# Kernel tuning notes

Measured on AMD Instinct MI355X. Metric: run time of the kernel, lower is better.

The kernel has to match this reference:

```python
import jax, jax.numpy as jnp
import numpy as np

N_NODES = 50000
N_EDGES = 800000
F_IN = 128
HEADS = 4
C_OUT = 16
NEG_SLOPE = 0.2


def setup_inputs() -> dict:
    key = jax.random.key(0)
    k1, k2, k3, k4, k5 = jax.random.split(key, 5)
    x = jax.random.normal(k1, (N_NODES, F_IN), dtype=jnp.float32)
    edge_index = jax.random.randint(k2, (2, N_EDGES), 0, N_NODES, dtype=jnp.int64)
    W = jax.random.normal(k3, (F_IN, HEADS * C_OUT), dtype=jnp.float32) * (1.0 / np.sqrt(F_IN))
    att_src = jax.random.normal(k4, (HEADS, C_OUT), dtype=jnp.float32) * (1.0 / np.sqrt(C_OUT))
    att_dst = jax.random.normal(k5, (HEADS, C_OUT), dtype=jnp.float32) * (1.0 / np.sqrt(C_OUT))
    bias = jnp.zeros((HEADS * C_OUT,), dtype=jnp.float32)
    return {"x": x, "edge_index": edge_index, "W": W,
            "att_src": att_src, "att_dst": att_dst, "bias": bias}


def reference(x, edge_index, W, att_src, att_dst, bias):
    N = x.shape[0]
    H, C = att_src.shape
    # PyG GATConv default: add self-loops
    loop = jnp.arange(N, dtype=edge_index.dtype)
    ei = jnp.concatenate([edge_index, jnp.stack([loop, loop])], axis=1)  # [2, E+N]
    src, dst = ei[0], ei[1]

    h = (x @ W).reshape(N, H, C)                      # [N, H, C]
    a_src = jnp.einsum('nhc,hc->nh', h, att_src)      # [N, H]
    a_dst = jnp.einsum('nhc,hc->nh', h, att_dst)      # [N, H]

    e = a_src[src] + a_dst[dst]                       # [E+N, H]
    e = jnp.where(e > 0, e, NEG_SLOPE * e)            # leaky_relu(0.2)

    # segment softmax over destination node (every segment has a self-loop)
    m = jax.ops.segment_max(e, dst, num_segments=N)   # [N, H]
    e = jnp.exp(e - m[dst])
    s = jax.ops.segment_sum(e, dst, num_segments=N)   # [N, H]
    alpha = e / (s[dst] + 1e-16)                      # [E+N, H]

    # scatter-aggregate weighted neighbor features
    out = jax.ops.segment_sum(h[src] * alpha[..., None], dst, num_segments=N)  # [N, H, C]
    out = out.reshape(N, H * C) + bias                # concat heads + bias
    return out, alpha
```

## Files before the change

### kernel.cpp

```cpp
#include <hip/hip_runtime.h>

#define N_NODES 50000
#define N_EDGES 800000
#define EN      (N_EDGES + N_NODES)
#define F_IN    128
#define HC      64
#define NEG_SLOPE 0.2f
#define NBUCK   196
#define BCAP    5120
#define P3_EPB  4096
#define LIN_BLOCKS 782
#define NBLK    196
#define RCAP    64
#define NSLOT   (NBLK * RCAP)
#define XPAD    136

typedef __attribute__((ext_vector_type(8))) short bf16x8;
typedef __attribute__((ext_vector_type(4))) float f32x4;

static __device__ __forceinline__ unsigned short f2bf(float f) {
    unsigned int b = __float_as_uint(f);
    return (unsigned short)((b + 0x7FFFu + ((b >> 16) & 1u)) >> 16);
}

__global__ __launch_bounds__(256) void
kA_linear_bin(const float* __restrict__ x, const float* __restrict__ W,
              const float* __restrict__ att_src, const float* __restrict__ att_dst,
              const int* __restrict__ ei,
              unsigned short* __restrict__ hbf, float* __restrict__ a_src,
              float* __restrict__ a_dst, int* __restrict__ bins,
              int* __restrict__ cntg) {
    __shared__ unsigned short xs[64][XPAD];
    __shared__ unsigned short wt[64][XPAD];
    __shared__ int bcnt_l[NBUCK];
    const int tid = threadIdx.x;

    if (blockIdx.x >= LIN_BLOCKS) {
        const int blk = blockIdx.x - LIN_BLOCKS;
        for (int i = tid; i < NBUCK; i += 256) bcnt_l[i] = 0;
        __syncthreads();
        const int base = blk * P3_EPB;
        #pragma unroll
        for (int j = 0; j < 16; ++j) {
            int i = base + j * 256 + tid;
            if (i < N_EDGES) {
                int sv = ei[i];
                int d  = ei[N_EDGES + i];
                int bk = d >> 8;
                int r  = atomicAdd(&bcnt_l[bk], 1);
                if (r < RCAP)
                    bins[(bk * NBLK + blk) * RCAP + r] = sv | ((d & 255) << 16);
            }
        }
        __syncthreads();
        for (int b = tid; b < NBUCK; b += 256)
            cntg[b * NBLK + blk] = min(bcnt_l[b], RCAP);
        return;
    }

    const int wv   = tid >> 6;
    const int l    = tid & 63;
    const int base = blockIdx.x * 64;
    const int c16  = l & 15;
    const int grp  = l >> 4;

    #pragma unroll
    for (int it = 0; it < 8; ++it) {
        int f  = it * 1024 + tid * 4;
        int k  = f >> 6;
        int cl = f & 63;
        float4 v = *(const float4*)(W + (size_t)k * HC + cl);
        wt[cl + 0][k] = f2bf(v.x);
        wt[cl + 1][k] = f2bf(v.y);
        wt[cl + 2][k] = f2bf(v.z);
        wt[cl + 3][k] = f2bf(v.w);
    }

    #pragma unroll
    for (int it = 0; it < 8; ++it) {
        int f   = it * 1024 + tid * 4;
        int row = f >> 7, k = f & 127;
        int gr  = base + row;
        float4 v = {0.f, 0.f, 0.f, 0.f};
        if (gr < N_NODES) v = *(const float4*)(x + (size_t)gr * F_IN + k);
        ushort4 u = {f2bf(v.x), f2bf(v.y), f2bf(v.z), f2bf(v.w)};
        *(ushort4*)(&xs[row][k]) = u;
    }
    __syncthreads();

    bf16x8 Bf[4][4];
    #pragma unroll
    for (int t = 0; t < 4; ++t)
        #pragma unroll
        for (int kk = 0; kk < 4; ++kk)
            Bf[t][kk] = *(const bf16x8*)(&wt[t * 16 + c16][kk * 32 + grp * 8]);

    const int r0 = wv * 16;
    f32x4 C[4];
    #pragma unroll
    for (int t = 0; t < 4; ++t) C[t] = (f32x4){0.f, 0.f, 0.f, 0.f};
    bf16x8 A[4];
    #pragma unroll
    for (int kk = 0; kk < 4; ++kk)
        A[kk] = *(const bf16x8*)(&xs[r0 + c16][kk * 32 + grp * 8]);
    #pragma unroll
    for (int t = 0; t < 4; ++t)
        #pragma unroll
        for (int kk = 0; kk < 4; ++kk)
            C[t] = __builtin_amdgcn_mfma_f32_16x16x32_bf16(A[kk], Bf[t][kk], C[t], 0, 0, 0);

    float asv[4], adv[4];
    #pragma unroll
    for (int t = 0; t < 4; ++t) {
        asv[t] = att_src[t * 16 + c16];
        adv[t] = att_dst[t * 16 + c16];
    }
    #pragma unroll
    for (int j = 0; j < 4; ++j) {
        const int row = base + r0 + grp * 4 + j;
        const bool ok = row < N_NODES;
        float4 ta, td;
        float* tap = (float*)&ta;
        float* tdp = (float*)&td;
        #pragma unroll
        for (int t = 0; t < 4; ++t) {
            const float hv = C[t][j];
            if (ok) hbf[(size_t)row * HC + t * 16 + c16] = f2bf(hv);
            float ts = hv * asv[t];
            float tdv = hv * adv[t];
            #pragma unroll
            for (int m = 1; m < 16; m <<= 1) {
                ts  += __shfl_xor(ts, m);
                tdv += __shfl_xor(tdv, m);
            }
            tap[t] = ts;
            tdp[t] = tdv;
        }
        if (ok && c16 == 0) {
            *(float4*)(a_src + row * 4) = ta;
            *(float4*)(a_dst + row * 4) = td;
        }
    }
}

__global__ __launch_bounds__(256) void
p4_csr(const int* __restrict__ bins, const int* __restrict__ cntg,
       int* __restrict__ row_info, int* __restrict__ srcs) {
    __shared__ int cntrow[NBLK];
    __shared__ int cnt[256], sm[256], cur[256];
    const int b = blockIdx.x, tid = threadIdx.x;
    const int node = (b << 8) + tid;

    if (tid < NBLK) cntrow[tid] = cntg[b * NBLK + tid];
    cnt[tid] = (node < N_NODES) ? 1 : 0;
    __syncthreads();

    const int* bb = bins + (size_t)b * NSLOT;
    for (int slot = tid; slot < NSLOT; slot += 256) {
        int blk = slot >> 6;
        int k   = slot & (RCAP - 1);
        if (k < cntrow[blk]) atomicAdd(&cnt[bb[slot] >> 16], 1);
    }
    __syncthreads();

    int v = cnt[tid];
    sm[tid] = v;
    __syncthreads();
    for (int off = 1; off < 256; off <<= 1) {
        int t = (tid >= off) ? sm[tid - off] : 0;
        __syncthreads();
        sm[tid] += t;
        __syncthreads();
    }
    const int ex = sm[tid] - v;
    const int sbase = b * BCAP;

    if (node < N_NODES) {
        row_info[node] = ((sbase + ex) << 8) | v;
        srcs[sbase + ex] = node;
    }
    cur[tid] = ex + 1;
    __syncthreads();
    for (int slot = tid; slot < NSLOT; slot += 256) {
        int blk = slot >> 6;
        int k   = slot & (RCAP - 1);
        if (k < cntrow[blk]) {
            int pv = bb[slot];
            int p  = atomicAdd(&cur[pv >> 16], 1);
            srcs[sbase + p] = pv & 0xFFFF;
        }
    }
}

__global__ __launch_bounds__(256) void
k_agg(const int* __restrict__ row_info, const int* __restrict__ srcs,
      const float* __restrict__ a_src, const float* __restrict__ a_dst,
      const unsigned int* __restrict__ hw,
      const float* __restrict__ bias, float* __restrict__ out,
      float* __restrict__ s_inv) {
    __shared__ int   s_lds[4][4][16];
    __shared__ float p_lds[4][4][16][4];

    const int tid  = threadIdx.x;
    const int wv   = tid >> 6;
    const int lane = tid & 63;
    const int g    = lane >> 4;
    const int l    = lane & 15;
    const int hd   = l >> 2;
    const int d    = blockIdx.x * 16 + wv * 4 + g;

    const int info   = row_info[d];
    const int begin  = info >> 8;
    const int cnt    = info & 255;
    const int nchunk = (cnt + 15) >> 4;
    const float4 ad  = *(const float4*)(a_dst + d * 4);

    float4 ps = {0.f, 0.f, 0.f, 0.f};
    float a0 = 0.f, a1 = 0.f, a2 = 0.f, a3 = 0.f;

    for (int c = 0; c < nchunk; ++c) {
        const int k0 = begin + c * 16;
        const int m  = min(16, begin + cnt - k0);
        const int s = srcs[k0 + (l < m ? l : m - 1)];
        float4 p = {0.f, 0.f, 0.f, 0.f};
        if (l < m) {
            float4 as = *(const float4*)(a_src + s * 4);
            float e0 = as.x + ad.x, e1 = as.y + ad.y, e2 = as.z + ad.z, e3 = as.w + ad.w;
            e0 = e0 > 0.f ? e0 : NEG_SLOPE * e0;
            e1 = e1 > 0.f ? e1 : NEG_SLOPE * e1;
            e2 = e2 > 0.f ? e2 : NEG_SLOPE * e2;
            e3 = e3 > 0.f ? e3 : NEG_SLOPE * e3;
            p.x = __expf(e0); p.y = __expf(e1); p.z = __expf(e2); p.w = __expf(e3);
            ps.x += p.x; ps.y += p.y; ps.z += p.z; ps.w += p.w;
        }
        s_lds[wv][g][l] = s;
        *(float4*)(&p_lds[wv][g][l][0]) = p;
        __threadfence_block();

        const int mp = (m + 3) & ~3;
        for (int e = 0; e < mp; e += 4) {
            int s0 = s_lds[wv][g][e + 0], s1 = s_lds[wv][g][e + 1];
            int s2 = s_lds[wv][g][e + 2], s3 = s_lds[wv][g][e + 3];
            float p0 = p_lds[wv][g][e + 0][hd], p1 = p_lds[wv][g][e + 1][hd];
            float p2 = p_lds[wv][g][e + 2][hd], p3 = p_lds[wv][g][e + 3][hd];
            uint2 u0 = *(const uint2*)(hw + (size_t)s0 * 32 + l * 2);
            uint2 u1 = *(const uint2*)(hw + (size_t)s1 * 32 + l * 2);
            uint2 u2 = *(const uint2*)(hw + (size_t)s2 * 32 + l * 2);
            uint2 u3 = *(const uint2*)(hw + (size_t)s3 * 32 + l * 2);
            a0 += __uint_as_float(u0.x << 16)         * p0;
            a1 += __uint_as_float(u0.x & 0xFFFF0000u) * p0;
            a2 += __uint_as_float(u0.y << 16)         * p0;
            a3 += __uint_as_float(u0.y & 0xFFFF0000u) * p0;
            a0 += __uint_as_float(u1.x << 16)         * p1;
            a1 += __uint_as_float(u1.x & 0xFFFF0000u) * p1;
            a2 += __uint_as_float(u1.y << 16)         * p1;
            a3 += __uint_as_float(u1.y & 0xFFFF0000u) * p1;
            a0 += __uint_as_float(u2.x << 16)         * p2;
            a1 += __uint_as_float(u2.x & 0xFFFF0000u) * p2;
            a2 += __uint_as_float(u2.y << 16)         * p2;
            a3 += __uint_as_float(u2.y & 0xFFFF0000u) * p2;
            a0 += __uint_as_float(u3.x << 16)         * p3;
            a1 += __uint_as_float(u3.x & 0xFFFF0000u) * p3;
            a2 += __uint_as_float(u3.y << 16)         * p3;
            a3 += __uint_as_float(u3.y & 0xFFFF0000u) * p3;
        }
        __threadfence_block();
    }

    #pragma unroll
    for (int mm = 1; mm < 16; mm <<= 1) {
        ps.x += __shfl_xor(ps.x, mm);
        ps.y += __shfl_xor(ps.y, mm);
        ps.z += __shfl_xor(ps.z, mm);
        ps.w += __shfl_xor(ps.w, mm);
    }
    const float4 inv = {1.f / (ps.x + 1e-16f), 1.f / (ps.y + 1e-16f),
                        1.f / (ps.z + 1e-16f), 1.f / (ps.w + 1e-16f)};
    if (l == 0) *(float4*)(s_inv + d * 4) = inv;

    const float invh = (hd == 0) ? inv.x : (hd == 1) ? inv.y : (hd == 2) ? inv.z : inv.w;
    float4 o;
    o.x = a0 * invh + bias[l * 4 + 0];
    o.y = a1 * invh + bias[l * 4 + 1];
    o.z = a2 * invh + bias[l * 4 + 2];
    o.w = a3 * invh + bias[l * 4 + 3];
    *(float4*)(out + (size_t)d * HC + l * 4) = o;
}

__global__ void k_alpha(const int* __restrict__ ei, const float* __restrict__ a_src,
                        const float* __restrict__ a_dst, const float* __restrict__ s_inv,
                        float* __restrict__ alpha_out) {
    int i2 = blockIdx.x * 256 + threadIdx.x;
    if (i2 >= EN / 2) return;
    const int i = i2 * 2;
    int s0, s1, d0, d1;
    if (i < N_EDGES) {
        int2 sp = *(const int2*)(ei + i);
        int2 dp = *(const int2*)(ei + N_EDGES + i);
        s0 = sp.x; s1 = sp.y; d0 = dp.x; d1 = dp.y;
    } else {
        s0 = d0 = i - N_EDGES;
        s1 = d1 = i + 1 - N_EDGES;
    }

    float4 as0 = *(const float4*)(a_src + s0 * 4);
    float4 ad0 = *(const float4*)(a_dst + d0 * 4);
    float4 iv0 = *(const float4*)(s_inv + d0 * 4);
    float4 as1 = *(const float4*)(a_src + s1 * 4);
    float4 ad1 = *(const float4*)(a_dst + d1 * 4);
    float4 iv1 = *(const float4*)(s_inv + d1 * 4);

    float e0, e1, e2, e3;
    e0 = as0.x + ad0.x; e1 = as0.y + ad0.y; e2 = as0.z + ad0.z; e3 = as0.w + ad0.w;
    e0 = e0 > 0.f ? e0 : NEG_SLOPE * e0;
    e1 = e1 > 0.f ? e1 : NEG_SLOPE * e1;
    e2 = e2 > 0.f ? e2 : NEG_SLOPE * e2;
    e3 = e3 > 0.f ? e3 : NEG_SLOPE * e3;
    float4 al0 = {__expf(e0) * iv0.x, __expf(e1) * iv0.y,
                  __expf(e2) * iv0.z, __expf(e3) * iv0.w};
    e0 = as1.x + ad1.x; e1 = as1.y + ad1.y; e2 = as1.z + ad1.z; e3 = as1.w + ad1.w;
    e0 = e0 > 0.f ? e0 : NEG_SLOPE * e0;
    e1 = e1 > 0.f ? e1 : NEG_SLOPE * e1;
    e2 = e2 > 0.f ? e2 : NEG_SLOPE * e2;
    e3 = e3 > 0.f ? e3 : NEG_SLOPE * e3;
    float4 al1 = {__expf(e0) * iv1.x, __expf(e1) * iv1.y,
                  __expf(e2) * iv1.z, __expf(e3) * iv1.w};

    *(float4*)(alpha_out + (size_t)i * 4)     = al0;
    *(float4*)(alpha_out + (size_t)i * 4 + 4) = al1;
}

extern "C" void kernel_launch(void* const* d_in, const int* in_sizes, int n_in,
                              void* d_out, int out_size, void* d_ws, size_t ws_size,
                              hipStream_t stream) {
    const float* x       = (const float*)d_in[0];
    const int*   ei      = (const int*)d_in[1];
    const float* W       = (const float*)d_in[2];
    const float* att_src = (const float*)d_in[3];
    const float* att_dst = (const float*)d_in[4];
    const float* bias    = (const float*)d_in[5];

    float* out       = (float*)d_out;
    float* alpha_out = (float*)d_out + (size_t)N_NODES * HC;

    char* ws = (char*)d_ws;
    size_t off = 0;
    unsigned short* hbf = (unsigned short*)(ws + off); off += (size_t)N_NODES * HC * 2;
    float* a_src   = (float*)(ws + off); off += (size_t)N_NODES * 4 * 4;
    float* a_dst   = (float*)(ws + off); off += (size_t)N_NODES * 4 * 4;
    float* s_inv   = (float*)(ws + off); off += (size_t)N_NODES * 4 * 4;
    int* row_info  = (int*)(ws + off);   off += (size_t)N_NODES * 4;
    int* srcs      = (int*)(ws + off);   off += (size_t)NBUCK * BCAP * 4;
    int* bins      = (int*)(ws + off);   off += (size_t)NBUCK * NSLOT * 4;
    int* cntg      = (int*)(ws + off);   off += (size_t)NBUCK * NBLK * 4;

    kA_linear_bin<<<LIN_BLOCKS + NBLK, 256, 0, stream>>>(x, W, att_src, att_dst, ei,
                                                         hbf, a_src, a_dst, bins, cntg);
    p4_csr<<<NBUCK, 256, 0, stream>>>(bins, cntg, row_info, srcs);
    k_agg<<<N_NODES / 16, 256, 0, stream>>>(row_info, srcs, a_src, a_dst,
                                            (const unsigned int*)hbf, bias, out, s_inv);
    k_alpha<<<(EN / 2 + 255) / 256, 256, 0, stream>>>(ei, a_src, a_dst, s_inv, alpha_out);
}
```

Measured before the change: 84.30 us.

## Replace binned CSR build with global-atomic CSR in cooperative megakernel

Drops the per-block binning plus LDS-atomic CSR construction and builds the CSR with global atomics instead: zero degrees, count them, scan per bucket, then scatter sources. The CSR build, aggregation and alpha phases are merged into one cooperative kernel with grid-wide syncs, which removes several kernel launches and the bins staging buffer. A fallback multi-kernel path runs if the cooperative launch fails. The costs are global atomic contention on degree and cursor arrays, grid syncs, a fixed 1024-block grid for the aggregation, and source order within each row that is no longer deterministic.

```diff
diff --git a/kernel.cpp b/kernel.cpp
--- a/kernel.cpp
+++ b/kernel.cpp
@@ -1,4 +1,7 @@
 #include <hip/hip_runtime.h>
+#include <hip/hip_cooperative_groups.h>
+
+namespace cg = cooperative_groups;
 
 #define N_NODES 50000
 #define N_EDGES 800000
@@ -8,12 +11,11 @@
 #define NEG_SLOPE 0.2f
 #define NBUCK   196
 #define BCAP    5120
-#define P3_EPB  4096
 #define LIN_BLOCKS 782
-#define NBLK    196
-#define RCAP    64
-#define NSLOT   (NBLK * RCAP)
 #define XPAD    136
+#define MEGA_GRID 1024
+#define NAGG    (N_NODES / 16)
+#define NPAIR   (EN / 2)
 
 typedef __attribute__((ext_vector_type(8))) short bf16x8;
 typedef __attribute__((ext_vector_type(4))) float f32x4;
@@ -24,39 +26,13 @@
 }
 
 __global__ __launch_bounds__(256) void
-kA_linear_bin(const float* __restrict__ x, const float* __restrict__ W,
-              const float* __restrict__ att_src, const float* __restrict__ att_dst,
-              const int* __restrict__ ei,
-              unsigned short* __restrict__ hbf, float* __restrict__ a_src,
-              float* __restrict__ a_dst, int* __restrict__ bins,
-              int* __restrict__ cntg) {
+kA_linear(const float* __restrict__ x, const float* __restrict__ W,
+          const float* __restrict__ att_src, const float* __restrict__ att_dst,
+          unsigned short* __restrict__ hbf, float* __restrict__ a_src,
+          float* __restrict__ a_dst) {
     __shared__ unsigned short xs[64][XPAD];
     __shared__ unsigned short wt[64][XPAD];
-    __shared__ int bcnt_l[NBUCK];
     const int tid = threadIdx.x;
-
-    if (blockIdx.x >= LIN_BLOCKS) {
-        const int blk = blockIdx.x - LIN_BLOCKS;
-        for (int i = tid; i < NBUCK; i += 256) bcnt_l[i] = 0;
-        __syncthreads();
-        const int base = blk * P3_EPB;
-        #pragma unroll
-        for (int j = 0; j < 16; ++j) {
-            int i = base + j * 256 + tid;
-            if (i < N_EDGES) {
-                int sv = ei[i];
-                int d  = ei[N_EDGES + i];
-                int bk = d >> 8;
-                int r  = atomicAdd(&bcnt_l[bk], 1);
-                if (r < RCAP)
-                    bins[(bk * NBLK + blk) * RCAP + r] = sv | ((d & 255) << 16);
-            }
-        }
-        __syncthreads();
-        for (int b = tid; b < NBUCK; b += 256)
-            cntg[b * NBLK + blk] = min(bcnt_l[b], RCAP);
-        return;
-    }
 
     const int wv   = tid >> 6;
     const int l    = tid & 63;
@@ -143,27 +119,28 @@
     }
 }
 
-__global__ __launch_bounds__(256) void
-p4_csr(const int* __restrict__ bins, const int* __restrict__ cntg,
-       int* __restrict__ row_info, int* __restrict__ srcs) {
-    __shared__ int cntrow[NBLK];
-    __shared__ int cnt[256], sm[256], cur[256];
-    const int b = blockIdx.x, tid = threadIdx.x;
+
+static __device__ __forceinline__ void
+phase_zero(int* __restrict__ deg, int gsz, int gtid) {
+    for (int i = gtid; i < N_NODES; i += gsz) deg[i] = 0;
+}
+
+static __device__ __forceinline__ void
+phase_count(const int* __restrict__ ei, int* __restrict__ deg, int gsz, int gtid) {
+    for (int e2 = gtid; e2 < N_EDGES / 2; e2 += gsz) {
+        int2 dp = *(const int2*)(ei + N_EDGES + e2 * 2);
+        atomicAdd(&deg[dp.x], 1);
+        atomicAdd(&deg[dp.y], 1);
+    }
+}
+
+static __device__ __forceinline__ void
+phase_scan(const int* __restrict__ deg, int* __restrict__ row_info,
+           int* __restrict__ srcs, int* __restrict__ cur, int* sm,
+           int b, int tid) {
     const int node = (b << 8) + tid;
-
-    if (tid < NBLK) cntrow[tid] = cntg[b * NBLK + tid];
-    cnt[tid] = (node < N_NODES) ? 1 : 0;
-    __syncthreads();
-
-    const int* bb = bins + (size_t)b * NSLOT;
-    for (int slot = tid; slot < NSLOT; slot += 256) {
-        int blk = slot >> 6;
-        int k   = slot & (RCAP - 1);
-        if (k < cntrow[blk]) atomicAdd(&cnt[bb[slot] >> 16], 1);
-    }
-    __syncthreads();
-
-    int v = cnt[tid];
+    int v = 0;
+    if (node < N_NODES) v = deg[node] + 1;
     sm[tid] = v;
     __syncthreads();
     for (int off = 1; off < 256; off <<= 1) {
@@ -174,160 +151,223 @@
     }
     const int ex = sm[tid] - v;
     const int sbase = b * BCAP;
-
     if (node < N_NODES) {
         row_info[node] = ((sbase + ex) << 8) | v;
         srcs[sbase + ex] = node;
-    }
-    cur[tid] = ex + 1;
-    __syncthreads();
-    for (int slot = tid; slot < NSLOT; slot += 256) {
-        int blk = slot >> 6;
-        int k   = slot & (RCAP - 1);
-        if (k < cntrow[blk]) {
-            int pv = bb[slot];
-            int p  = atomicAdd(&cur[pv >> 16], 1);
-            srcs[sbase + p] = pv & 0xFFFF;
-        }
-    }
-}
-
-__global__ __launch_bounds__(256) void
-k_agg(const int* __restrict__ row_info, const int* __restrict__ srcs,
-      const float* __restrict__ a_src, const float* __restrict__ a_dst,
-      const unsigned int* __restrict__ hw,
-      const float* __restrict__ bias, float* __restrict__ out,
-      float* __restrict__ s_inv) {
-    __shared__ int   s_lds[4][4][16];
-    __shared__ float p_lds[4][4][16][4];
-
-    const int tid  = threadIdx.x;
+        cur[node] = sbase + ex + 1;
+    }
+}
+
+static __device__ __forceinline__ void
+phase_scatter(const int* __restrict__ ei, int* __restrict__ cur,
+              int* __restrict__ srcs, int gsz, int gtid) {
+    for (int e2 = gtid; e2 < N_EDGES / 2; e2 += gsz) {
+        int2 sp = *(const int2*)(ei + e2 * 2);
+        int2 dp = *(const int2*)(ei + N_EDGES + e2 * 2);
+        int p0 = atomicAdd(&cur[dp.x], 1);
+        srcs[p0] = sp.x;
+        int p1 = atomicAdd(&cur[dp.y], 1);
+        srcs[p1] = sp.y;
+    }
+}
+
+static __device__ __forceinline__ void
+phase_agg(const int* __restrict__ row_info, const int* __restrict__ srcs,
+          const float* __restrict__ a_src, const float* __restrict__ a_dst,
+          const unsigned int* __restrict__ hw, const float* __restrict__ bias,
+          float* __restrict__ out, float* __restrict__ s_inv,
+          int (*s_lds)[4][16], float (*p_lds)[4][16][4],
+          int nblk, int bid, int tid) {
     const int wv   = tid >> 6;
     const int lane = tid & 63;
     const int g    = lane >> 4;
     const int l    = lane & 15;
     const int hd   = l >> 2;
-    const int d    = blockIdx.x * 16 + wv * 4 + g;
-
-    const int info   = row_info[d];
-    const int begin  = info >> 8;
-    const int cnt    = info & 255;
-    const int nchunk = (cnt + 15) >> 4;
-    const float4 ad  = *(const float4*)(a_dst + d * 4);
-
-    float4 ps = {0.f, 0.f, 0.f, 0.f};
-    float a0 = 0.f, a1 = 0.f, a2 = 0.f, a3 = 0.f;
-
-    for (int c = 0; c < nchunk; ++c) {
-        const int k0 = begin + c * 16;
-        const int m  = min(16, begin + cnt - k0);
-        const int s = srcs[k0 + (l < m ? l : m - 1)];
-        float4 p = {0.f, 0.f, 0.f, 0.f};
-        if (l < m) {
-            float4 as = *(const float4*)(a_src + s * 4);
-            float e0 = as.x + ad.x, e1 = as.y + ad.y, e2 = as.z + ad.z, e3 = as.w + ad.w;
-            e0 = e0 > 0.f ? e0 : NEG_SLOPE * e0;
-            e1 = e1 > 0.f ? e1 : NEG_SLOPE * e1;
-            e2 = e2 > 0.f ? e2 : NEG_SLOPE * e2;
-            e3 = e3 > 0.f ? e3 : NEG_SLOPE * e3;
-            p.x = __expf(e0); p.y = __expf(e1); p.z = __expf(e2); p.w = __expf(e3);
-            ps.x += p.x; ps.y += p.y; ps.z += p.z; ps.w += p.w;
+
+    for (int u = bid; u < NAGG; u += nblk) {
+        const int d = u * 16 + wv * 4 + g;
+
+        const int info   = row_info[d];
+        const int begin  = info >> 8;
+        const int cnt    = info & 255;
+        const int nchunk = (cnt + 15) >> 4;
+        const float4 ad  = *(const float4*)(a_dst + d * 4);
+
+        float4 ps = {0.f, 0.f, 0.f, 0.f};
+        float a0 = 0.f, a1 = 0.f, a2 = 0.f, a3 = 0.f;
+
+        for (int c = 0; c < nchunk; ++c) {
+            const int k0 = begin + c * 16;
+            const int m  = min(16, begin + cnt - k0);
+            const int s = srcs[k0 + (l < m ? l : m - 1)];
+            float4 p = {0.f, 0.f, 0.f, 0.f};
+            if (l < m) {
+                float4 as = *(const float4*)(a_src + s * 4);
+                float e0 = as.x + ad.x, e1 = as.y + ad.y, e2 = as.z + ad.z, e3 = as.w + ad.w;
+                e0 = e0 > 0.f ? e0 : NEG_SLOPE * e0;
+                e1 = e1 > 0.f ? e1 : NEG_SLOPE * e1;
+                e2 = e2 > 0.f ? e2 : NEG_SLOPE * e2;
+                e3 = e3 > 0.f ? e3 : NEG_SLOPE * e3;
+                p.x = __expf(e0); p.y = __expf(e1); p.z = __expf(e2); p.w = __expf(e3);
+                ps.x += p.x; ps.y += p.y; ps.z += p.z; ps.w += p.w;
+            }
+            s_lds[wv][g][l] = s;
+            *(float4*)(&p_lds[wv][g][l][0]) = p;
+            __threadfence_block();
+
+            const int mp = (m + 3) & ~3;
+            for (int e = 0; e < mp; e += 4) {
+                int s0 = s_lds[wv][g][e + 0], s1 = s_lds[wv][g][e + 1];
+                int s2 = s_lds[wv][g][e + 2], s3 = s_lds[wv][g][e + 3];
+                float p0 = p_lds[wv][g][e + 0][hd], p1 = p_lds[wv][g][e + 1][hd];
+                float p2 = p_lds[wv][g][e + 2][hd], p3 = p_lds[wv][g][e + 3][hd];
+                uint2 u0 = *(const uint2*)(hw + (size_t)s0 * 32 + l * 2);
+                uint2 u1 = *(const uint2*)(hw + (size_t)s1 * 32 + l * 2);
+                uint2 u2 = *(const uint2*)(hw + (size_t)s2 * 32 + l * 2);
+                uint2 u3 = *(const uint2*)(hw + (size_t)s3 * 32 + l * 2);
+                a0 += __uint_as_float(u0.x << 16)         * p0;
+                a1 += __uint_as_float(u0.x & 0xFFFF0000u) * p0;
+                a2 += __uint_as_float(u0.y << 16)         * p0;
+                a3 += __uint_as_float(u0.y & 0xFFFF0000u) * p0;
+                a0 += __uint_as_float(u1.x << 16)         * p1;
+                a1 += __uint_as_float(u1.x & 0xFFFF0000u) * p1;
+                a2 += __uint_as_float(u1.y << 16)         * p1;
+                a3 += __uint_as_float(u1.y & 0xFFFF0000u) * p1;
+                a0 += __uint_as_float(u2.x << 16)         * p2;
+                a1 += __uint_as_float(u2.x & 0xFFFF0000u) * p2;
+                a2 += __uint_as_float(u2.y << 16)         * p2;
+                a3 += __uint_as_float(u2.y & 0xFFFF0000u) * p2;
+                a0 += __uint_as_float(u3.x << 16)         * p3;
+                a1 += __uint_as_float(u3.x & 0xFFFF0000u) * p3;
+                a2 += __uint_as_float(u3.y << 16)         * p3;
+                a3 += __uint_as_float(u3.y & 0xFFFF0000u) * p3;
+            }
+            __threadfence_block();
         }
-        s_lds[wv][g][l] = s;
-        *(float4*)(&p_lds[wv][g][l][0]) = p;
-        __threadfence_block();
-
-        const int mp = (m + 3) & ~3;
-        for (int e = 0; e < mp; e += 4) {
-            int s0 = s_lds[wv][g][e + 0], s1 = s_lds[wv][g][e + 1];
-            int s2 = s_lds[wv][g][e + 2], s3 = s_lds[wv][g][e + 3];
-            float p0 = p_lds[wv][g][e + 0][hd], p1 = p_lds[wv][g][e + 1][hd];
-            float p2 = p_lds[wv][g][e + 2][hd], p3 = p_lds[wv][g][e + 3][hd];
-            uint2 u0 = *(const uint2*)(hw + (size_t)s0 * 32 + l * 2);
-            uint2 u1 = *(const uint2*)(hw + (size_t)s1 * 32 + l * 2);
-            uint2 u2 = *(const uint2*)(hw + (size_t)s2 * 32 + l * 2);
-            uint2 u3 = *(const uint2*)(hw + (size_t)s3 * 32 + l * 2);
-            a0 += __uint_as_float(u0.x << 16)         * p0;
-            a1 += __uint_as_float(u0.x & 0xFFFF0000u) * p0;
-            a2 += __uint_as_float(u0.y << 16)         * p0;
-            a3 += __uint_as_float(u0.y & 0xFFFF0000u) * p0;
-            a0 += __uint_as_float(u1.x << 16)         * p1;
-            a1 += __uint_as_float(u1.x & 0xFFFF0000u) * p1;
-            a2 += __uint_as_float(u1.y << 16)         * p1;
-            a3 += __uint_as_float(u1.y & 0xFFFF0000u) * p1;
-            a0 += __uint_as_float(u2.x << 16)         * p2;
-            a1 += __uint_as_float(u2.x & 0xFFFF0000u) * p2;
-            a2 += __uint_as_float(u2.y << 16)         * p2;
-            a3 += __uint_as_float(u2.y & 0xFFFF0000u) * p2;
-            a0 += __uint_as_float(u3.x << 16)         * p3;
-            a1 += __uint_as_float(u3.x & 0xFFFF0000u) * p3;
-            a2 += __uint_as_float(u3.y << 16)         * p3;
-            a3 += __uint_as_float(u3.y & 0xFFFF0000u) * p3;
+
+        #pragma unroll
+        for (int mm = 1; mm < 16; mm <<= 1) {
+            ps.x += __shfl_xor(ps.x, mm);
+            ps.y += __shfl_xor(ps.y, mm);
+            ps.z += __shfl_xor(ps.z, mm);
+            ps.w += __shfl_xor(ps.w, mm);
         }
-        __threadfence_block();
-    }
-
-    #pragma unroll
-    for (int mm = 1; mm < 16; mm <<= 1) {
-        ps.x += __shfl_xor(ps.x, mm);
-        ps.y += __shfl_xor(ps.y, mm);
-        ps.z += __shfl_xor(ps.z, mm);
-        ps.w += __shfl_xor(ps.w, mm);
-    }
-    const float4 inv = {1.f / (ps.x + 1e-16f), 1.f / (ps.y + 1e-16f),
-                        1.f / (ps.z + 1e-16f), 1.f / (ps.w + 1e-16f)};
-    if (l == 0) *(float4*)(s_inv + d * 4) = inv;
-
-    const float invh = (hd == 0) ? inv.x : (hd == 1) ? inv.y : (hd == 2) ? inv.z : inv.w;
-    float4 o;
-    o.x = a0 * invh + bias[l * 4 + 0];
-    o.y = a1 * invh + bias[l * 4 + 1];
-    o.z = a2 * invh + bias[l * 4 + 2];
-    o.w = a3 * invh + bias[l * 4 + 3];
-    *(float4*)(out + (size_t)d * HC + l * 4) = o;
-}
-
-__global__ void k_alpha(const int* __restrict__ ei, const float* __restrict__ a_src,
-                        const float* __restrict__ a_dst, const float* __restrict__ s_inv,
-                        float* __restrict__ alpha_out) {
-    int i2 = blockIdx.x * 256 + threadIdx.x;
-    if (i2 >= EN / 2) return;
-    const int i = i2 * 2;
-    int s0, s1, d0, d1;
-    if (i < N_EDGES) {
-        int2 sp = *(const int2*)(ei + i);
-        int2 dp = *(const int2*)(ei + N_EDGES + i);
-        s0 = sp.x; s1 = sp.y; d0 = dp.x; d1 = dp.y;
-    } else {
-        s0 = d0 = i - N_EDGES;
-        s1 = d1 = i + 1 - N_EDGES;
-    }
-
-    float4 as0 = *(const float4*)(a_src + s0 * 4);
-    float4 ad0 = *(const float4*)(a_dst + d0 * 4);
-    float4 iv0 = *(const float4*)(s_inv + d0 * 4);
-    float4 as1 = *(const float4*)(a_src + s1 * 4);
-    float4 ad1 = *(const float4*)(a_dst + d1 * 4);
-    float4 iv1 = *(const float4*)(s_inv + d1 * 4);
-
-    float e0, e1, e2, e3;
-    e0 = as0.x + ad0.x; e1 = as0.y + ad0.y; e2 = as0.z + ad0.z; e3 = as0.w + ad0.w;
-    e0 = e0 > 0.f ? e0 : NEG_SLOPE * e0;
-    e1 = e1 > 0.f ? e1 : NEG_SLOPE * e1;
-    e2 = e2 > 0.f ? e2 : NEG_SLOPE * e2;
-    e3 = e3 > 0.f ? e3 : NEG_SLOPE * e3;
-    float4 al0 = {__expf(e0) * iv0.x, __expf(e1) * iv0.y,
-                  __expf(e2) * iv0.z, __expf(e3) * iv0.w};
-    e0 = as1.x + ad1.x; e1 = as1.y + ad1.y; e2 = as1.z + ad1.z; e3 = as1.w + ad1.w;
-    e0 = e0 > 0.f ? e0 : NEG_SLOPE * e0;
-    e1 = e1 > 0.f ? e1 : NEG_SLOPE * e1;
-    e2 = e2 > 0.f ? e2 : NEG_SLOPE * e2;
-    e3 = e3 > 0.f ? e3 : NEG_SLOPE * e3;
-    float4 al1 = {__expf(e0) * iv1.x, __expf(e1) * iv1.y,
-                  __expf(e2) * iv1.z, __expf(e3) * iv1.w};
-
-    *(float4*)(alpha_out + (size_t)i * 4)     = al0;
-    *(float4*)(alpha_out + (size_t)i * 4 + 4) = al1;
+        const float4 inv = {1.f / (ps.x + 1e-16f), 1.f / (ps.y + 1e-16f),
+                            1.f / (ps.z + 1e-16f), 1.f / (ps.w + 1e-16f)};
+        if (l == 0) *(float4*)(s_inv + d * 4) = inv;
+
+        const float invh = (hd == 0) ? inv.x : (hd == 1) ? inv.y : (hd == 2) ? inv.z : inv.w;
+        float4 o;
+        o.x = a0 * invh + bias[l * 4 + 0];
+        o.y = a1 * invh + bias[l * 4 + 1];
+        o.z = a2 * invh + bias[l * 4 + 2];
+        o.w = a3 * invh + bias[l * 4 + 3];
+        *(float4*)(out + (size_t)d * HC + l * 4) = o;
+    }
+}
+
+static __device__ __forceinline__ void
+phase_alpha(const int* __restrict__ ei, const float* __restrict__ a_src,
+            const float* __restrict__ a_dst, const float* __restrict__ s_inv,
+            float* __restrict__ alpha_out, int gsz, int gtid) {
+    for (int i2 = gtid; i2 < NPAIR; i2 += gsz) {
+        const int i = i2 * 2;
+        int s0, s1, d0, d1;
+        if (i < N_EDGES) {
+            int2 sp = *(const int2*)(ei + i);
+            int2 dp = *(const int2*)(ei + N_EDGES + i);
+            s0 = sp.x; s1 = sp.y; d0 = dp.x; d1 = dp.y;
+        } else {
+            s0 = d0 = i - N_EDGES;
+            s1 = d1 = i + 1 - N_EDGES;
+        }
+
+        float4 as0 = *(const float4*)(a_src + s0 * 4);
+        float4 ad0 = *(const float4*)(a_dst + d0 * 4);
+        float4 iv0 = *(const float4*)(s_inv + d0 * 4);
+        float4 as1 = *(const float4*)(a_src + s1 * 4);
+        float4 ad1 = *(const float4*)(a_dst + d1 * 4);
+        float4 iv1 = *(const float4*)(s_inv + d1 * 4);
+
+        float e0, e1, e2, e3;
+        e0 = as0.x + ad0.x; e1 = as0.y + ad0.y; e2 = as0.z + ad0.z; e3 = as0.w + ad0.w;
+        e0 = e0 > 0.f ? e0 : NEG_SLOPE * e0;
+        e1 = e1 > 0.f ? e1 : NEG_SLOPE * e1;
+        e2 = e2 > 0.f ? e2 : NEG_SLOPE * e2;
+        e3 = e3 > 0.f ? e3 : NEG_SLOPE * e3;
+        float4 al0 = {__expf(e0) * iv0.x, __expf(e1) * iv0.y,
+                      __expf(e2) * iv0.z, __expf(e3) * iv0.w};
+        e0 = as1.x + ad1.x; e1 = as1.y + ad1.y; e2 = as1.z + ad1.z; e3 = as1.w + ad1.w;
+        e0 = e0 > 0.f ? e0 : NEG_SLOPE * e0;
+        e1 = e1 > 0.f ? e1 : NEG_SLOPE * e1;
+        e2 = e2 > 0.f ? e2 : NEG_SLOPE * e2;
+        e3 = e3 > 0.f ? e3 : NEG_SLOPE * e3;
+        float4 al1 = {__expf(e0) * iv1.x, __expf(e1) * iv1.y,
+                      __expf(e2) * iv1.z, __expf(e3) * iv1.w};
+
+        *(float4*)(alpha_out + (size_t)i * 4)     = al0;
+        *(float4*)(alpha_out + (size_t)i * 4 + 4) = al1;
+    }
+}
+
+__global__ __launch_bounds__(256, 4) void
+mega(const int* __restrict__ ei, const float* __restrict__ a_src,
+     const float* __restrict__ a_dst, const unsigned int* __restrict__ hw,
+     const float* __restrict__ bias, float* __restrict__ out,
+     float* __restrict__ s_inv, int* __restrict__ deg, int* __restrict__ cur,
+     int* __restrict__ row_info, int* __restrict__ srcs,
+     float* __restrict__ alpha_out) {
+    __shared__ int   sm[256];
+    __shared__ int   s_lds[4][4][16];
+    __shared__ float p_lds[4][4][16][4];
+
+    cg::grid_group grid = cg::this_grid();
+    const int tid  = threadIdx.x;
+    const int bid  = blockIdx.x;
+    const int gsz  = (int)gridDim.x << 8;
+    const int gtid = (bid << 8) + tid;
+
+    phase_zero(deg, gsz, gtid);
+    grid.sync();
+    phase_count(ei, deg, gsz, gtid);
+    grid.sync();
+    if (bid < NBUCK) phase_scan(deg, row_info, srcs, cur, sm, bid, tid);
+    grid.sync();
+    phase_scatter(ei, cur, srcs, gsz, gtid);
+    grid.sync();
+    phase_agg(row_info, srcs, a_src, a_dst, hw, bias, out, s_inv,
+              s_lds, p_lds, (int)gridDim.x, bid, tid);
+    grid.sync();
+    phase_alpha(ei, a_src, a_dst, s_inv, alpha_out, gsz, gtid);
+}
+
+__global__ __launch_bounds__(256) void k_zero(int* deg) {
+    phase_zero(deg, gridDim.x << 8, (blockIdx.x << 8) + threadIdx.x);
+}
+__global__ __launch_bounds__(256) void k_count(const int* ei, int* deg) {
+    phase_count(ei, deg, gridDim.x << 8, (blockIdx.x << 8) + threadIdx.x);
+}
+__global__ __launch_bounds__(256) void
+k_scan(const int* deg, int* row_info, int* srcs, int* cur) {
+    __shared__ int sm[256];
+    phase_scan(deg, row_info, srcs, cur, sm, blockIdx.x, threadIdx.x);
+}
+__global__ __launch_bounds__(256) void k_scatter(const int* ei, int* cur, int* srcs) {
+    phase_scatter(ei, cur, srcs, gridDim.x << 8, (blockIdx.x << 8) + threadIdx.x);
+}
+__global__ __launch_bounds__(256) void
+k_aggf(const int* row_info, const int* srcs, const float* a_src, const float* a_dst,
+       const unsigned int* hw, const float* bias, float* out, float* s_inv) {
+    __shared__ int   s_lds[4][4][16];
+    __shared__ float p_lds[4][4][16][4];
+    phase_agg(row_info, srcs, a_src, a_dst, hw, bias, out, s_inv,
+              s_lds, p_lds, gridDim.x, blockIdx.x, threadIdx.x);
+}
+__global__ __launch_bounds__(256) void
+k_alphaf(const int* ei, const float* a_src, const float* a_dst,
+         const float* s_inv, float* alpha_out) {
+    phase_alpha(ei, a_src, a_dst, s_inv, alpha_out,
+                gridDim.x << 8, (blockIdx.x << 8) + threadIdx.x);
 }
 
 extern "C" void kernel_launch(void* const* d_in, const int* in_sizes, int n_in,
@@ -351,13 +391,29 @@
     float* s_inv   = (float*)(ws + off); off += (size_t)N_NODES * 4 * 4;
     int* row_info  = (int*)(ws + off);   off += (size_t)N_NODES * 4;
     int* srcs      = (int*)(ws + off);   off += (size_t)NBUCK * BCAP * 4;
-    int* bins      = (int*)(ws + off);   off += (size_t)NBUCK * NSLOT * 4;
-    int* cntg      = (int*)(ws + off);   off += (size_t)NBUCK * NBLK * 4;
-
-    kA_linear_bin<<<LIN_BLOCKS + NBLK, 256, 0, stream>>>(x, W, att_src, att_dst, ei,
-                                                         hbf, a_src, a_dst, bins, cntg);
-    p4_csr<<<NBUCK, 256, 0, stream>>>(bins, cntg, row_info, srcs);
-    k_agg<<<N_NODES / 16, 256, 0, stream>>>(row_info, srcs, a_src, a_dst,
-                                            (const unsigned int*)hbf, bias, out, s_inv);
-    k_alpha<<<(EN / 2 + 255) / 256, 256, 0, stream>>>(ei, a_src, a_dst, s_inv, alpha_out);
-}
+    int* deg       = (int*)(ws + off);   off += (size_t)N_NODES * 4;
+    int* cur       = (int*)(ws + off);   off += (size_t)N_NODES * 4;
+
+    kA_linear<<<LIN_BLOCKS, 256, 0, stream>>>(x, W, att_src, att_dst, hbf, a_src, a_dst);
+
+    static int coop_ok = -1;
+    if (coop_ok != 0) {
+        const unsigned int* hw = (const unsigned int*)hbf;
+        void* args[12] = {
+            (void*)&ei, (void*)&a_src, (void*)&a_dst, (void*)&hw, (void*)&bias,
+            (void*)&out, (void*)&s_inv, (void*)&deg, (void*)&cur,
+            (void*)&row_info, (void*)&srcs, (void*)&alpha_out};
+        hipError_t e = hipLaunchCooperativeKernel((void*)mega, dim3(MEGA_GRID),
+                                                  dim3(256), args, 0, stream);
+        coop_ok = (e == hipSuccess) ? 1 : 0;
+    }
+    if (coop_ok == 0) {
+        k_zero<<<196, 256, 0, stream>>>(deg);
+        k_count<<<782, 256, 0, stream>>>(ei, deg);
+        k_scan<<<NBUCK, 256, 0, stream>>>(deg, row_info, srcs, cur);
+        k_scatter<<<782, 256, 0, stream>>>(ei, cur, srcs);
+        k_aggf<<<NAGG, 256, 0, stream>>>(row_info, srcs, a_src, a_dst,
+                                         (const unsigned int*)hbf, bias, out, s_inv);
+        k_alphaf<<<(NPAIR + 255) / 256, 256, 0, stream>>>(ei, a_src, a_dst, s_inv, alpha_out);
+    }
+}
```

After: 147.1 us. 74.5% more time.

## Fold attention vectors into GEMM and compact bin scan in CSR build

Applied to the files above, without the earlier changes.

In the linear kernel, the attention projections W·att_src and W·att_dst are precomputed as 8 extra output columns, so one extra MFMA tile produces a_src/a_dst directly. This replaces the per-row shuffle reductions, at the cost of computing those columns in bf16. In the CSR kernel, a prefix sum over per-block bin counts lets threads iterate only over valid entries, using a binary search per entry. The loaded values are cached in registers between the counting and placement passes, which avoids scanning all 12544 slots twice and re-reading bins. The register array assumes at most 5120 entries per bucket, and the bf16 rounding of the folded attention weights changes numerics slightly.

```diff
diff --git a/kernel.cpp b/kernel.cpp
--- a/kernel.cpp
+++ b/kernel.cpp
@@ -31,7 +31,7 @@
               float* __restrict__ a_dst, int* __restrict__ bins,
               int* __restrict__ cntg) {
     __shared__ unsigned short xs[64][XPAD];
-    __shared__ unsigned short wt[64][XPAD];
+    __shared__ unsigned short wt[80][XPAD];
     __shared__ int bcnt_l[NBUCK];
     const int tid = threadIdx.x;
 
@@ -86,19 +86,40 @@
         ushort4 u = {f2bf(v.x), f2bf(v.y), f2bf(v.z), f2bf(v.w)};
         *(ushort4*)(&xs[row][k]) = u;
     }
-    __syncthreads();
-
-    bf16x8 Bf[4][4];
-    #pragma unroll
-    for (int t = 0; t < 4; ++t)
+
+    {
+        const int wk = tid >> 1;
+        const int wo = (tid & 1) * 4;
+        const float* wrow = W + (size_t)wk * HC;
+        #pragma unroll
+        for (int oo = 0; oo < 4; ++oo) {
+            const int o = wo + oo;
+            const int h = o & 3;
+            const float* av = (o < 4) ? (att_src + h * 16) : (att_dst + h * 16);
+            float a = 0.f;
+            #pragma unroll
+            for (int c = 0; c < 16; c += 4) {
+                float4 w4 = *(const float4*)(wrow + h * 16 + c);
+                float4 a4 = *(const float4*)(av + c);
+                a += w4.x * a4.x + w4.y * a4.y + w4.z * a4.z + w4.w * a4.w;
+            }
+            wt[64 + o][wk] = f2bf(a);
+        }
+    }
+    __syncthreads();
+
+    bf16x8 Bf[5][4];
+    #pragma unroll
+    for (int t = 0; t < 5; ++t)
         #pragma unroll
         for (int kk = 0; kk < 4; ++kk)
             Bf[t][kk] = *(const bf16x8*)(&wt[t * 16 + c16][kk * 32 + grp * 8]);
 
     const int r0 = wv * 16;
-    f32x4 C[4];
+    f32x4 C[4], C4;
     #pragma unroll
     for (int t = 0; t < 4; ++t) C[t] = (f32x4){0.f, 0.f, 0.f, 0.f};
+    C4 = (f32x4){0.f, 0.f, 0.f, 0.f};
     bf16x8 A[4];
     #pragma unroll
     for (int kk = 0; kk < 4; ++kk)
@@ -108,37 +129,19 @@
         #pragma unroll
         for (int kk = 0; kk < 4; ++kk)
             C[t] = __builtin_amdgcn_mfma_f32_16x16x32_bf16(A[kk], Bf[t][kk], C[t], 0, 0, 0);
-
-    float asv[4], adv[4];
-    #pragma unroll
-    for (int t = 0; t < 4; ++t) {
-        asv[t] = att_src[t * 16 + c16];
-        adv[t] = att_dst[t * 16 + c16];
-    }
+    #pragma unroll
+    for (int kk = 0; kk < 4; ++kk)
+        C4 = __builtin_amdgcn_mfma_f32_16x16x32_bf16(A[kk], Bf[4][kk], C4, 0, 0, 0);
+
     #pragma unroll
     for (int j = 0; j < 4; ++j) {
         const int row = base + r0 + grp * 4 + j;
-        const bool ok = row < N_NODES;
-        float4 ta, td;
-        float* tap = (float*)&ta;
-        float* tdp = (float*)&td;
-        #pragma unroll
-        for (int t = 0; t < 4; ++t) {
-            const float hv = C[t][j];
-            if (ok) hbf[(size_t)row * HC + t * 16 + c16] = f2bf(hv);
-            float ts = hv * asv[t];
-            float tdv = hv * adv[t];
+        if (row < N_NODES) {
             #pragma unroll
-            for (int m = 1; m < 16; m <<= 1) {
-                ts  += __shfl_xor(ts, m);
-                tdv += __shfl_xor(tdv, m);
-            }
-            tap[t] = ts;
-            tdp[t] = tdv;
-        }
-        if (ok && c16 == 0) {
-            *(float4*)(a_src + row * 4) = ta;
-            *(float4*)(a_dst + row * 4) = td;
+            for (int t = 0; t < 4; ++t)
+                hbf[(size_t)row * HC + t * 16 + c16] = f2bf(C[t][j]);
+            if (c16 < 4)      a_src[row * 4 + c16]       = C4[j];
+            else if (c16 < 8) a_dst[row * 4 + (c16 - 4)] = C4[j];
         }
     }
 }
@@ -146,20 +149,36 @@
 __global__ __launch_bounds__(256) void
 p4_csr(const int* __restrict__ bins, const int* __restrict__ cntg,
        int* __restrict__ row_info, int* __restrict__ srcs) {
-    __shared__ int cntrow[NBLK];
+    __shared__ int psum[256];
     __shared__ int cnt[256], sm[256], cur[256];
     const int b = blockIdx.x, tid = threadIdx.x;
     const int node = (b << 8) + tid;
 
-    if (tid < NBLK) cntrow[tid] = cntg[b * NBLK + tid];
+    psum[tid] = (tid < NBLK) ? cntg[b * NBLK + tid] : 0;
     cnt[tid] = (node < N_NODES) ? 1 : 0;
     __syncthreads();
-
+    for (int off = 1; off < 256; off <<= 1) {
+        int t = (tid >= off) ? psum[tid - off] : 0;
+        __syncthreads();
+        psum[tid] += t;
+        __syncthreads();
+    }
+    const int T = psum[255];
     const int* bb = bins + (size_t)b * NSLOT;
-    for (int slot = tid; slot < NSLOT; slot += 256) {
-        int blk = slot >> 6;
-        int k   = slot & (RCAP - 1);
-        if (k < cntrow[blk]) atomicAdd(&cnt[bb[slot] >> 16], 1);
+
+    int pvs[20];
+    #pragma unroll
+    for (int it = 0; it < 20; ++it) {
+        const int i = tid + it * 256;
+        if (i < T) {
+            int lo = 0, hi = NBLK - 1;
+            while (lo < hi) { int mid = (lo + hi) >> 1;
+                              if (psum[mid] > i) hi = mid; else lo = mid + 1; }
+            const int k  = i - (lo ? psum[lo - 1] : 0);
+            const int pv = bb[lo * RCAP + k];
+            pvs[it] = pv;
+            atomicAdd(&cnt[pv >> 16], 1);
+        }
     }
     __syncthreads();
 
@@ -181,12 +200,12 @@
     }
     cur[tid] = ex + 1;
     __syncthreads();
-    for (int slot = tid; slot < NSLOT; slot += 256) {
-        int blk = slot >> 6;
-        int k   = slot & (RCAP - 1);
-        if (k < cntrow[blk]) {
-            int pv = bb[slot];
-            int p  = atomicAdd(&cur[pv >> 16], 1);
+    #pragma unroll
+    for (int it = 0; it < 20; ++it) {
+        const int i = tid + it * 256;
+        if (i < T) {
+            const int pv = pvs[it];
+            const int p  = atomicAdd(&cur[pv >> 16], 1);
             srcs[sbase + p] = pv & 0xFFFF;
         }
     }
```

Result: faster. 80.93 us (-4.0%).
